# Kernel tuning notes

Measured on AMD Instinct MI355X. Metric: run time of the kernel, lower is better.

Reference implementation:

```python
import jax, jax.numpy as jnp
import numpy as np

B, S, H = 2, 2048, 1024
NH = 16
HD = H // NH
SCALE = 1.0 / np.sqrt(HD).astype(np.float32)


def setup_inputs() -> dict:
    key = jax.random.key(0)
    ks = jax.random.split(key, 7)
    lim = 1.0 / np.sqrt(H)  # lecun-ish init scale for linear weights
    return {
        "query": jax.random.normal(ks[0], (B, S, H), dtype=jnp.float32),
        "key_in": jax.random.normal(ks[1], (B, S, H), dtype=jnp.float32),
        "value": jax.random.normal(ks[2], (B, S, H), dtype=jnp.float32),
        "attention_mask": jnp.ones((B, S), dtype=jnp.int32),
        "Wq": jax.random.uniform(ks[3], (H, H), jnp.float32, -lim, lim),
        "Wk": jax.random.uniform(ks[4], (H, H), jnp.float32, -lim, lim),
        "Wv": jax.random.uniform(ks[5], (H, H), jnp.float32, -lim, lim),
        "Wo": jax.random.uniform(ks[6], (H, H), jnp.float32, -lim, lim),
    }


def reference(query, key_in, value, attention_mask, Wq, Wk, Wv, Wo):
    b, s, _ = query.shape
    # projections (no bias)
    q = (query @ Wq).reshape(b, s, NH, HD).transpose(0, 2, 1, 3)  # [b,h,s,d]
    k = (key_in @ Wk).reshape(b, s, NH, HD).transpose(0, 2, 1, 3)
    v = (value @ Wv).reshape(b, s, NH, HD).transpose(0, 2, 1, 3)

    scores = jnp.einsum("bhqd,bhkd->bhqk", q, k) * SCALE  # [b,h,s,s]
    mask = attention_mask[:, None, None, :]  # broadcast over heads & query pos
    scores = jnp.where(mask == 0, -1e9, scores)
    attn = jax.nn.softmax(scores, axis=-1)

    ctx = jnp.einsum("bhqk,bhkd->bhqd", attn, v)
    ctx = ctx.transpose(0, 2, 1, 3).reshape(b, s, H)
    out = ctx @ Wo
    return out, jnp.mean(attn, axis=1)
```

## Files before the change

### kernel.cpp

```cpp
#include <hip/hip_runtime.h>
#include <stdint.h>

#define BB 2
#define SS 2048
#define HH 1024
#define NHEAD 16
#define HDIM 64

constexpr int   BSROWS = BB * SS;
constexpr float SCALE  = 0.125f;
constexpr float LOG2E  = 1.4426950408889634f;
constexpr float SL     = SCALE * LOG2E;

typedef __bf16 bf16;
typedef __attribute__((ext_vector_type(8))) __bf16 bf16x8;
typedef __attribute__((ext_vector_type(4))) __bf16 bf16x4;
typedef __attribute__((ext_vector_type(4))) float  f32x4;

#define MFMA16(a, b, c) __builtin_amdgcn_mfma_f32_16x16x32_bf16((a), (b), (c), 0, 0, 0)

__device__ __forceinline__ void gload_lds16(const void* g, void* l) {
  __builtin_amdgcn_global_load_lds((const __attribute__((address_space(1))) void*)g,
                                   (__attribute__((address_space(3))) void*)l, 16, 0, 0);
}

__global__ __launch_bounds__(256) void cvt_in(const float* __restrict__ q, const float* __restrict__ k,
                                              const float* __restrict__ v, const int* __restrict__ mask,
                                              bf16* __restrict__ xq, bf16* __restrict__ xk,
                                              bf16* __restrict__ xv, float* __restrict__ bias2) {
  int i = blockIdx.x * 256 + threadIdx.x;
  int e = i * 4;
  f32x4 a = *(const f32x4*)(q + e);
  f32x4 b = *(const f32x4*)(k + e);
  f32x4 c = *(const f32x4*)(v + e);
  *(bf16x4*)(xq + e) = __builtin_convertvector(a, bf16x4);
  *(bf16x4*)(xk + e) = __builtin_convertvector(b, bf16x4);
  *(bf16x4*)(xv + e) = __builtin_convertvector(c, bf16x4);
  if (i < BB * SS) bias2[i] = mask[i] ? 0.0f : -1e9f * LOG2E;
}

__global__ __launch_bounds__(256) void cvt_wt(const float* __restrict__ Wq, const float* __restrict__ Wk,
                                              const float* __restrict__ Wv, const float* __restrict__ Wo,
                                              bf16* __restrict__ Wt) {
  __shared__ float tile[32][33];
  int z = blockIdx.z;
  const float* W = (z == 0) ? Wq : (z == 1) ? Wk : (z == 2) ? Wv : Wo;
  bf16* out = Wt + (size_t)z * HH * HH;
  int bx = blockIdx.x * 32, by = blockIdx.y * 32;
  int tx = threadIdx.x, ty = threadIdx.y;
#pragma unroll
  for (int j = 0; j < 32; j += 8)
    tile[ty + j][tx] = W[(size_t)(by + ty + j) * HH + bx + tx];
  __syncthreads();
#pragma unroll
  for (int j = 0; j < 32; j += 8)
    out[(size_t)(bx + ty + j) * HH + by + tx] = (bf16)tile[tx][ty + j];
}

__global__ __launch_bounds__(256) void gemm128(const bf16* __restrict__ Abase, const bf16* __restrict__ Btbase,
                                               bf16* __restrict__ Qo, bf16* __restrict__ Ko,
                                               bf16* __restrict__ Vto, float* __restrict__ outF, int mode) {
  int id  = blockIdx.x + 8 * blockIdx.y + 256 * blockIdx.z;
  int nwg = 256 * gridDim.z;
  int sw  = (id & 7) * (nwg >> 3) + (id >> 3);
  int bx  = sw & 7, by = (sw >> 3) & 31, bz = sw >> 8;

  int zmode = (mode < 0) ? bz : mode;
  const bf16* A  = Abase  + (mode < 0 ? (size_t)bz * BSROWS * HH : 0);
  const bf16* Bt = Btbase + (mode < 0 ? (size_t)bz * HH * HH : 0);

  __shared__ __align__(16) bf16 lA[2][128 * 32];
  __shared__ __align__(16) bf16 lB[2][128 * 32];

  int t = threadIdx.x;
  int w = t >> 6, l = t & 63, lg = l >> 4, lr = l & 15;
  int m0 = by * 128, n0 = bx * 128;
  int wr = (w >> 1) * 64, wc = (w & 1) * 64;

  f32x4 zero4 = {0.f, 0.f, 0.f, 0.f};
  f32x4 acc[4][4];
#pragma unroll
  for (int i = 0; i < 4; i++)
#pragma unroll
    for (int j = 0; j < 4; j++) acc[i][j] = zero4;

#pragma unroll
  for (int i = 0; i < 2; i++) {
    int idx = i * 256 + t;
    gload_lds16(A  + (size_t)(m0 + (idx >> 2)) * HH + (idx & 3) * 8, &lA[0][(i * 256 + w * 64) * 8]);
    gload_lds16(Bt + (size_t)(n0 + (idx >> 2)) * HH + (idx & 3) * 8, &lB[0][(i * 256 + w * 64) * 8]);
  }
  __syncthreads();

  for (int kt = 0; kt < 32; kt++) {
    int cur = kt & 1;
    if (kt < 31) {
      int kn = (kt + 1) * 32;
#pragma unroll
      for (int i = 0; i < 2; i++) {
        int idx = i * 256 + t;
        gload_lds16(A  + (size_t)(m0 + (idx >> 2)) * HH + kn + (idx & 3) * 8, &lA[cur ^ 1][(i * 256 + w * 64) * 8]);
        gload_lds16(Bt + (size_t)(n0 + (idx >> 2)) * HH + kn + (idx & 3) * 8, &lB[cur ^ 1][(i * 256 + w * 64) * 8]);
      }
    }
    bf16x8 af[4], bq[4];
#pragma unroll
    for (int mi = 0; mi < 4; mi++) af[mi] = *(const bf16x8*)&lA[cur][(wr + mi * 16 + lr) * 32 + lg * 8];
#pragma unroll
    for (int ni = 0; ni < 4; ni++) bq[ni] = *(const bf16x8*)&lB[cur][(wc + ni * 16 + lr) * 32 + lg * 8];
#pragma unroll
    for (int mi = 0; mi < 4; mi++)
#pragma unroll
      for (int ni = 0; ni < 4; ni++)
        acc[mi][ni] = MFMA16(af[mi], bq[ni], acc[mi][ni]);
    __syncthreads();
  }

#pragma unroll
  for (int mi = 0; mi < 4; mi++) {
    int row0 = m0 + wr + mi * 16 + lg * 4;
#pragma unroll
    for (int ni = 0; ni < 4; ni++) {
      int col = n0 + wc + ni * 16 + lr;
      if (zmode == 3) {
#pragma unroll
        for (int r = 0; r < 4; r++) outF[(size_t)(row0 + r) * HH + col] = acc[mi][ni][r];
      } else if (zmode == 2) {
        int b = row0 >> 11, s0 = row0 & (SS - 1);
        int h = col >> 6, d = col & 63;
        bf16x4 pk;
#pragma unroll
        for (int r = 0; r < 4; r++) pk[r] = (bf16)acc[mi][ni][r];
        *(bf16x4*)&Vto[((size_t)(b * NHEAD + h) * HDIM + d) * SS + s0] = pk;
      } else {
        bf16* dst = (zmode == 0) ? Qo : Ko;
        int h = col >> 6, d = col & 63;
#pragma unroll
        for (int r = 0; r < 4; r++) {
          int row = row0 + r;
          int b = row >> 11, s = row & (SS - 1);
          dst[((size_t)(b * NHEAD + h) * SS + s) * HDIM + d] = (bf16)acc[mi][ni][r];
        }
      }
    }
  }
}

__global__ __launch_bounds__(256, 2) void attn_pv(const bf16* __restrict__ Q, const bf16* __restrict__ K,
                                                  const bf16* __restrict__ Vt, const float* __restrict__ bias2,
                                                  float* __restrict__ invl, bf16* __restrict__ ctx) {
  int id = blockIdx.x + 16 * blockIdx.y + 256 * blockIdx.z;
  int sw = (id & 7) * 64 + (id >> 3);
  int b = sw >> 8, h = (sw >> 4) & 15, q0 = (sw & 15) * 128;
  int t = threadIdx.x, w = t >> 6, l = t & 63, lg = l >> 4, lr = l & 15;
  size_t hb = ((size_t)b * NHEAD + h) * SS;
  const bf16* Qh = Q + hb * HDIM;
  const bf16* Kh = K + hb * HDIM;
  const bf16* Vh = Vt + ((size_t)b * NHEAD + h) * HDIM * SS;
  const float* biasb = bias2 + b * SS;

  __shared__ __align__(16) bf16 sK[2][64][72];
  __shared__ __align__(16) bf16 sV[2][64][72];
  __shared__ __align__(16) bf16 lp[4][2][32][72];

  int r0 = t >> 3, c0 = (t & 7) * 8;
  bf16x8 kreg[2], vreg[2];

  int qa = q0 + w * 32;
  int rowa = qa + lr, rowb = qa + 16 + lr;
  bf16x8 qf0a = *(const bf16x8*)&Qh[(size_t)rowa * HDIM + lg * 8];
  bf16x8 qf1a = *(const bf16x8*)&Qh[(size_t)rowa * HDIM + 32 + lg * 8];
  bf16x8 qf0b = *(const bf16x8*)&Qh[(size_t)rowb * HDIM + lg * 8];
  bf16x8 qf1b = *(const bf16x8*)&Qh[(size_t)rowb * HDIM + 32 + lg * 8];

  f32x4 zero4 = {0.f, 0.f, 0.f, 0.f};
  f32x4 lacca = zero4, laccb = zero4;
  f32x4 ctxa[4], ctxb[4];
#pragma unroll
  for (int nd = 0; nd < 4; nd++) { ctxa[nd] = zero4; ctxb[nd] = zero4; }
  bf16x8 vh[2][4];

#pragma unroll
  for (int i = 0; i < 2; i++) {
    int row = i * 32 + r0;
    kreg[i] = *(const bf16x8*)&Kh[(size_t)row * HDIM + c0];
    vreg[i] = *(const bf16x8*)&Vh[(size_t)row * SS + c0];
  }
#pragma unroll
  for (int i = 0; i < 2; i++) {
    int row = i * 32 + r0;
    *(bf16x8*)&sK[0][row][c0] = kreg[i];
    *(bf16x8*)&sV[0][row][c0] = vreg[i];
  }
  __syncthreads();

  for (int kt = 0; kt < 32; kt++) {
    int k0 = kt * 64, cur = kt & 1, prev = cur ^ 1;
    if (kt < 31) {
      int kn = k0 + 64;
#pragma unroll
      for (int i = 0; i < 2; i++) {
        int row = i * 32 + r0;
        kreg[i] = *(const bf16x8*)&Kh[(size_t)(kn + row) * HDIM + c0];
        vreg[i] = *(const bf16x8*)&Vh[(size_t)row * SS + kn + c0];
      }
    }
    if (kt > 0) {
#pragma unroll
      for (int kk = 0; kk < 2; kk++) {
        bf16x8 paa = *(const bf16x8*)&lp[w][prev][lr][kk * 32 + lg * 8];
        bf16x8 pab = *(const bf16x8*)&lp[w][prev][16 + lr][kk * 32 + lg * 8];
#pragma unroll
        for (int nd = 0; nd < 4; nd++) {
          ctxa[nd] = MFMA16(paa, vh[kk][nd], ctxa[nd]);
          ctxb[nd] = MFMA16(pab, vh[kk][nd], ctxb[nd]);
        }
      }
    }
    f32x4 acca[4], accb[4];
#pragma unroll
    for (int ni = 0; ni < 4; ni++) {
      const bf16* kp = &sK[cur][ni * 16 + lr][lg * 8];
      bf16x8 kf0 = *(const bf16x8*)kp;
      bf16x8 kf1 = *(const bf16x8*)(kp + 32);
      acca[ni] = MFMA16(kf1, qf1a, MFMA16(kf0, qf0a, zero4));
      accb[ni] = MFMA16(kf1, qf1b, MFMA16(kf0, qf0b, zero4));
    }
#pragma unroll
    for (int kk = 0; kk < 2; kk++)
#pragma unroll
      for (int nd = 0; nd < 4; nd++)
        vh[kk][nd] = *(const bf16x8*)&sV[cur][nd * 16 + lr][kk * 32 + lg * 8];
    f32x4 pa4[4], pb4[4];
#pragma unroll
    for (int ni = 0; ni < 4; ni++) {
      f32x4 bv = *(const f32x4*)&biasb[k0 + ni * 16 + lg * 4];
      f32x4 za = acca[ni] * SL + bv;
      f32x4 zb = accb[ni] * SL + bv;
#pragma unroll
      for (int r = 0; r < 4; r++) {
        pa4[ni][r] = __builtin_amdgcn_exp2f(za[r]);
        pb4[ni][r] = __builtin_amdgcn_exp2f(zb[r]);
      }
    }
    lacca += (pa4[0] + pa4[1]) + (pa4[2] + pa4[3]);
    laccb += (pb4[0] + pb4[1]) + (pb4[2] + pb4[3]);
#pragma unroll
    for (int ni = 0; ni < 4; ni++) {
      *(bf16x4*)&lp[w][cur][lr][ni * 16 + lg * 4]      = __builtin_convertvector(pa4[ni], bf16x4);
      *(bf16x4*)&lp[w][cur][16 + lr][ni * 16 + lg * 4] = __builtin_convertvector(pb4[ni], bf16x4);
    }
    if (kt < 31) {
#pragma unroll
      for (int i = 0; i < 2; i++) {
        int row = i * 32 + r0;
        *(bf16x8*)&sK[prev][row][c0] = kreg[i];
        *(bf16x8*)&sV[prev][row][c0] = vreg[i];
      }
      __syncthreads();
    }
  }

#pragma unroll
  for (int kk = 0; kk < 2; kk++) {
    bf16x8 paa = *(const bf16x8*)&lp[w][1][lr][kk * 32 + lg * 8];
    bf16x8 pab = *(const bf16x8*)&lp[w][1][16 + lr][kk * 32 + lg * 8];
#pragma unroll
    for (int nd = 0; nd < 4; nd++) {
      ctxa[nd] = MFMA16(paa, vh[kk][nd], ctxa[nd]);
      ctxb[nd] = MFMA16(pab, vh[kk][nd], ctxb[nd]);
    }
  }

  float lsa = (lacca[0] + lacca[1]) + (lacca[2] + lacca[3]);
  float lsb = (laccb[0] + laccb[1]) + (laccb[2] + laccb[3]);
  lsa += __shfl_xor(lsa, 16); lsa += __shfl_xor(lsa, 32);
  lsb += __shfl_xor(lsb, 16); lsb += __shfl_xor(lsb, 32);
  float ila = 1.0f / lsa, ilb = 1.0f / lsb;
  f32x4 ilva, ilvb;
#pragma unroll
  for (int r = 0; r < 4; r++) { ilva[r] = __shfl(ila, lg * 4 + r); ilvb[r] = __shfl(ilb, lg * 4 + r); }
#pragma unroll
  for (int nd = 0; nd < 4; nd++)
#pragma unroll
    for (int r = 0; r < 4; r++) {
      int ra = qa + lg * 4 + r, rb = qa + 16 + lg * 4 + r;
      ctx[(size_t)(b * SS + ra) * HH + h * HDIM + nd * 16 + lr] = (bf16)(ctxa[nd][r] * ilva[r]);
      ctx[(size_t)(b * SS + rb) * HH + h * HDIM + nd * 16 + lr] = (bf16)(ctxb[nd][r] * ilvb[r]);
    }
  if (l < 16) {
    invl[hb + qa + l]      = ila;
    invl[hb + qa + 16 + l] = ilb;
  }
}

__global__ __launch_bounds__(256, 4) void attn_mean(const bf16* __restrict__ Q, const bf16* __restrict__ K,
                                                    const float* __restrict__ bias2,
                                                    const float* __restrict__ invl, float* __restrict__ meanOut) {
  int id = blockIdx.x + 16 * blockIdx.y + 512 * blockIdx.z;
  int sw = (id & 7) * 128 + (id >> 3);
  int b = sw >> 9, kc0 = ((sw >> 4) & 31) * 64, q0 = (sw & 15) * 128;
  int t = threadIdx.x, w = t >> 6, l = t & 63, lg = l >> 4, lr = l & 15;
  const float* biasb = bias2 + b * SS;
  __shared__ __align__(16) bf16 sK[2][64][64];

  int rloc = l >> 3;
  int csw  = (l & 7) ^ (rloc & 7);
  int swz  = lr & 7;

  int qa = q0 + w * 32;
  int rowa = qa + lr, rowb = qa + 16 + lr;

  f32x4 bv[4];
#pragma unroll
  for (int ni = 0; ni < 4; ni++) bv[ni] = *(const f32x4*)&biasb[kc0 + ni * 16 + lg * 4];

  f32x4 zero4 = {0.f, 0.f, 0.f, 0.f};
  f32x4 macca[4], maccb[4];
#pragma unroll
  for (int ni = 0; ni < 4; ni++) { macca[ni] = zero4; maccb[ni] = zero4; }

  bf16x8 qf0a, qf1a, qf0b, qf1b;
  float ila, ilb;
  {
    const bf16* Kh0 = K + ((size_t)b * NHEAD) * SS * HDIM;
#pragma unroll
    for (int i = 0; i < 2; i++) {
      int rs = w * 16 + i * 8;
      gload_lds16(Kh0 + (size_t)(kc0 + rs + rloc) * HDIM + csw * 8, &sK[0][rs][0]);
    }
    const bf16* Qh0 = Q + ((size_t)b * NHEAD) * SS * HDIM;
    qf0a = *(const bf16x8*)&Qh0[(size_t)rowa * HDIM + lg * 8];
    qf1a = *(const bf16x8*)&Qh0[(size_t)rowa * HDIM + 32 + lg * 8];
    qf0b = *(const bf16x8*)&Qh0[(size_t)rowb * HDIM + lg * 8];
    qf1b = *(const bf16x8*)&Qh0[(size_t)rowb * HDIM + 32 + lg * 8];
    size_t hb0 = (size_t)b * NHEAD * SS;
    ila = invl[hb0 + rowa] * (1.0f / NHEAD);
    ilb = invl[hb0 + rowb] * (1.0f / NHEAD);
  }
  __syncthreads();

  for (int h = 0; h < NHEAD; h++) {
    int cur = h & 1;
    bf16x8 qn0a, qn1a, qn0b, qn1b;
    float ina = 0.f, inb = 0.f;
    if (h < NHEAD - 1) {
      size_t hbn = ((size_t)b * NHEAD + h + 1) * SS;
      const bf16* Khn = K + hbn * HDIM;
#pragma unroll
      for (int i = 0; i < 2; i++) {
        int rs = w * 16 + i * 8;
        gload_lds16(Khn + (size_t)(kc0 + rs + rloc) * HDIM + csw * 8, &sK[cur ^ 1][rs][0]);
      }
      const bf16* Qhn = Q + hbn * HDIM;
      qn0a = *(const bf16x8*)&Qhn[(size_t)rowa * HDIM + lg * 8];
      qn1a = *(const bf16x8*)&Qhn[(size_t)rowa * HDIM + 32 + lg * 8];
      qn0b = *(const bf16x8*)&Qhn[(size_t)rowb * HDIM + lg * 8];
      qn1b = *(const bf16x8*)&Qhn[(size_t)rowb * HDIM + 32 + lg * 8];
      ina = invl[hbn + rowa] * (1.0f / NHEAD);
      inb = invl[hbn + rowb] * (1.0f / NHEAD);
    }
#pragma unroll
    for (int ni = 0; ni < 4; ni++) {
      bf16x8 kf0 = *(const bf16x8*)&sK[cur][ni * 16 + lr][(lg ^ swz) * 8];
      bf16x8 kf1 = *(const bf16x8*)&sK[cur][ni * 16 + lr][((4 + lg) ^ swz) * 8];
      f32x4 acca = MFMA16(kf1, qf1a, MFMA16(kf0, qf0a, zero4));
      f32x4 accb = MFMA16(kf1, qf1b, MFMA16(kf0, qf0b, zero4));
      f32x4 za = acca * SL + bv[ni];
      f32x4 zb = accb * SL + bv[ni];
#pragma unroll
      for (int r = 0; r < 4; r++) {
        macca[ni][r] += __builtin_amdgcn_exp2f(za[r]) * ila;
        maccb[ni][r] += __builtin_amdgcn_exp2f(zb[r]) * ilb;
      }
    }
    if (h < NHEAD - 1) {
      qf0a = qn0a; qf1a = qn1a; qf0b = qn0b; qf1b = qn1b;
      ila = ina; ilb = inb;
      __syncthreads();
    }
  }
  float* meanB = meanOut + (size_t)b * SS * SS;
#pragma unroll
  for (int ni = 0; ni < 4; ni++) {
    *(f32x4*)&meanB[(size_t)rowa * SS + kc0 + ni * 16 + lg * 4] = macca[ni];
    *(f32x4*)&meanB[(size_t)rowb * SS + kc0 + ni * 16 + lg * 4] = maccb[ni];
  }
}

extern "C" void kernel_launch(void* const* d_in, const int* in_sizes, int n_in,
                              void* d_out, int out_size, void* d_ws, size_t ws_size,
                              hipStream_t stream) {
  const float* query  = (const float*)d_in[0];
  const float* key_in = (const float*)d_in[1];
  const float* value  = (const float*)d_in[2];
  const int*   mask   = (const int*)d_in[3];
  const float* Wq     = (const float*)d_in[4];
  const float* Wk     = (const float*)d_in[5];
  const float* Wv     = (const float*)d_in[6];
  const float* Wo     = (const float*)d_in[7];

  char* ws = (char*)d_ws;
  bf16*  Xb    = (bf16*)(ws);
  bf16*  Wt    = (bf16*)(ws + 25165824);
  bf16*  Qb    = (bf16*)(ws + 33554432);
  bf16*  Kb    = (bf16*)(ws + 41943040);
  bf16*  Vtb   = (bf16*)(ws + 50331648);
  float* invlb = (float*)(ws + 58982400);
  float* biasb = (float*)(ws + 59244544);
  bf16*  ctxb  = Xb;

  float* outF  = (float*)d_out;
  float* meanF = outF + (size_t)BB * SS * HH;

  cvt_in<<<4096, 256, 0, stream>>>(query, key_in, value, mask,
                                   Xb, Xb + 4194304, Xb + 8388608, biasb);
  cvt_wt<<<dim3(32, 32, 4), dim3(32, 8), 0, stream>>>(Wq, Wk, Wv, Wo, Wt);
  gemm128<<<dim3(8, 32, 3), 256, 0, stream>>>(Xb, Wt, Qb, Kb, Vtb, nullptr, -1);
  attn_pv<<<dim3(16, 16, 2), 256, 0, stream>>>(Qb, Kb, Vtb, biasb, invlb, ctxb);
  attn_mean<<<dim3(16, 32, 2), 256, 0, stream>>>(Qb, Kb, biasb, invlb, meanF);
  gemm128<<<dim3(8, 32, 1), 256, 0, stream>>>(ctxb, Wt + 3 * (size_t)HH * HH,
                                              nullptr, nullptr, nullptr, outF, 3);
}
```

Before: 178.6 us.

## Give each attention wave 64 query rows with 2 waves per block

```diff
diff --git a/kernel.cpp b/kernel.cpp
--- a/kernel.cpp
+++ b/kernel.cpp
@@ -146,9 +146,9 @@
   }
 }
 
-__global__ __launch_bounds__(256, 2) void attn_pv(const bf16* __restrict__ Q, const bf16* __restrict__ K,
-                                                  const bf16* __restrict__ Vt, const float* __restrict__ bias2,
-                                                  float* __restrict__ invl, bf16* __restrict__ ctx) {
+__global__ __launch_bounds__(128) void attn_pv(const bf16* __restrict__ Q, const bf16* __restrict__ K,
+                                               const bf16* __restrict__ Vt, const float* __restrict__ bias2,
+                                               float* __restrict__ invl, bf16* __restrict__ ctx) {
   int id = blockIdx.x + 16 * blockIdx.y + 256 * blockIdx.z;
   int sw = (id & 7) * 64 + (id >> 3);
   int b = sw >> 8, h = (sw >> 4) & 15, q0 = (sw & 15) * 128;
@@ -161,36 +161,44 @@
 
   __shared__ __align__(16) bf16 sK[2][64][72];
   __shared__ __align__(16) bf16 sV[2][64][72];
-  __shared__ __align__(16) bf16 lp[4][2][32][72];
+  __shared__ __align__(16) bf16 lp[2][2][64][72];
 
   int r0 = t >> 3, c0 = (t & 7) * 8;
-  bf16x8 kreg[2], vreg[2];
-
-  int qa = q0 + w * 32;
-  int rowa = qa + lr, rowb = qa + 16 + lr;
-  bf16x8 qf0a = *(const bf16x8*)&Qh[(size_t)rowa * HDIM + lg * 8];
-  bf16x8 qf1a = *(const bf16x8*)&Qh[(size_t)rowa * HDIM + 32 + lg * 8];
-  bf16x8 qf0b = *(const bf16x8*)&Qh[(size_t)rowb * HDIM + lg * 8];
-  bf16x8 qf1b = *(const bf16x8*)&Qh[(size_t)rowb * HDIM + 32 + lg * 8];
+  bf16x8 kreg[4], vreg[4];
+
+  int qa = q0 + w * 64;
+  bf16x8 qf0[4], qf1[4];
+#pragma unroll
+  for (int c = 0; c < 4; c++) {
+    int rowc = qa + c * 16 + lr;
+    qf0[c] = *(const bf16x8*)&Qh[(size_t)rowc * HDIM + lg * 8];
+    qf1[c] = *(const bf16x8*)&Qh[(size_t)rowc * HDIM + 32 + lg * 8];
+  }
 
   f32x4 zero4 = {0.f, 0.f, 0.f, 0.f};
-  f32x4 lacca = zero4, laccb = zero4;
-  f32x4 ctxa[4], ctxb[4];
-#pragma unroll
-  for (int nd = 0; nd < 4; nd++) { ctxa[nd] = zero4; ctxb[nd] = zero4; }
+  f32x4 lacc[4];
+  f32x4 ctxc[4][4];
+#pragma unroll
+  for (int c = 0; c < 4; c++) {
+    lacc[c] = zero4;
+#pragma unroll
+    for (int nd = 0; nd < 4; nd++) ctxc[c][nd] = zero4;
+  }
   bf16x8 vh[2][4];
 
 #pragma unroll
-  for (int i = 0; i < 2; i++) {
-    int row = i * 32 + r0;
-    kreg[i] = *(const bf16x8*)&Kh[(size_t)row * HDIM + c0];
-    vreg[i] = *(const bf16x8*)&Vh[(size_t)row * SS + c0];
-  }
-#pragma unroll
-  for (int i = 0; i < 2; i++) {
-    int row = i * 32 + r0;
-    *(bf16x8*)&sK[0][row][c0] = kreg[i];
-    *(bf16x8*)&sV[0][row][c0] = vreg[i];
+  for (int i = 0; i < 4; i++) {
+    int idx = i * 128 + t;
+    int row = idx >> 3, col = (idx & 7) * 8;
+    kreg[i] = *(const bf16x8*)&Kh[(size_t)row * HDIM + col];
+    vreg[i] = *(const bf16x8*)&Vh[(size_t)row * SS + col];
+  }
+#pragma unroll
+  for (int i = 0; i < 4; i++) {
+    int idx = i * 128 + t;
+    int row = idx >> 3, col = (idx & 7) * 8;
+    *(bf16x8*)&sK[0][row][col] = kreg[i];
+    *(bf16x8*)&sV[0][row][col] = vreg[i];
   }
   __syncthreads();
 
@@ -199,98 +207,90 @@
     if (kt < 31) {
       int kn = k0 + 64;
 #pragma unroll
-      for (int i = 0; i < 2; i++) {
-        int row = i * 32 + r0;
-        kreg[i] = *(const bf16x8*)&Kh[(size_t)(kn + row) * HDIM + c0];
-        vreg[i] = *(const bf16x8*)&Vh[(size_t)row * SS + kn + c0];
+      for (int i = 0; i < 4; i++) {
+        int idx = i * 128 + t;
+        int row = idx >> 3, col = (idx & 7) * 8;
+        kreg[i] = *(const bf16x8*)&Kh[(size_t)(kn + row) * HDIM + col];
+        vreg[i] = *(const bf16x8*)&Vh[(size_t)row * SS + kn + col];
       }
     }
     if (kt > 0) {
 #pragma unroll
-      for (int kk = 0; kk < 2; kk++) {
-        bf16x8 paa = *(const bf16x8*)&lp[w][prev][lr][kk * 32 + lg * 8];
-        bf16x8 pab = *(const bf16x8*)&lp[w][prev][16 + lr][kk * 32 + lg * 8];
-#pragma unroll
-        for (int nd = 0; nd < 4; nd++) {
-          ctxa[nd] = MFMA16(paa, vh[kk][nd], ctxa[nd]);
-          ctxb[nd] = MFMA16(pab, vh[kk][nd], ctxb[nd]);
+      for (int kk = 0; kk < 2; kk++)
+#pragma unroll
+        for (int c = 0; c < 4; c++) {
+          bf16x8 pac = *(const bf16x8*)&lp[w][prev][c * 16 + lr][kk * 32 + lg * 8];
+#pragma unroll
+          for (int nd = 0; nd < 4; nd++)
+            ctxc[c][nd] = MFMA16(pac, vh[kk][nd], ctxc[c][nd]);
         }
-      }
-    }
-    f32x4 acca[4], accb[4];
+    }
+    f32x4 acc[4][4];
 #pragma unroll
     for (int ni = 0; ni < 4; ni++) {
       const bf16* kp = &sK[cur][ni * 16 + lr][lg * 8];
       bf16x8 kf0 = *(const bf16x8*)kp;
       bf16x8 kf1 = *(const bf16x8*)(kp + 32);
-      acca[ni] = MFMA16(kf1, qf1a, MFMA16(kf0, qf0a, zero4));
-      accb[ni] = MFMA16(kf1, qf1b, MFMA16(kf0, qf0b, zero4));
+#pragma unroll
+      for (int c = 0; c < 4; c++)
+        acc[c][ni] = MFMA16(kf1, qf1[c], MFMA16(kf0, qf0[c], zero4));
     }
 #pragma unroll
     for (int kk = 0; kk < 2; kk++)
 #pragma unroll
       for (int nd = 0; nd < 4; nd++)
         vh[kk][nd] = *(const bf16x8*)&sV[cur][nd * 16 + lr][kk * 32 + lg * 8];
-    f32x4 pa4[4], pb4[4];
 #pragma unroll
     for (int ni = 0; ni < 4; ni++) {
       f32x4 bv = *(const f32x4*)&biasb[k0 + ni * 16 + lg * 4];
-      f32x4 za = acca[ni] * SL + bv;
-      f32x4 zb = accb[ni] * SL + bv;
+#pragma unroll
+      for (int c = 0; c < 4; c++) {
+        f32x4 z = acc[c][ni] * SL + bv;
+        f32x4 p;
+#pragma unroll
+        for (int r = 0; r < 4; r++) p[r] = __builtin_amdgcn_exp2f(z[r]);
+        lacc[c] += p;
+        *(bf16x4*)&lp[w][cur][c * 16 + lr][ni * 16 + lg * 4] = __builtin_convertvector(p, bf16x4);
+      }
+    }
+    if (kt < 31) {
+#pragma unroll
+      for (int i = 0; i < 4; i++) {
+        int idx = i * 128 + t;
+        int row = idx >> 3, col = (idx & 7) * 8;
+        *(bf16x8*)&sK[prev][row][col] = kreg[i];
+        *(bf16x8*)&sV[prev][row][col] = vreg[i];
+      }
+      __syncthreads();
+    }
+  }
+
+#pragma unroll
+  for (int kk = 0; kk < 2; kk++)
+#pragma unroll
+    for (int c = 0; c < 4; c++) {
+      bf16x8 pac = *(const bf16x8*)&lp[w][1][c * 16 + lr][kk * 32 + lg * 8];
+#pragma unroll
+      for (int nd = 0; nd < 4; nd++)
+        ctxc[c][nd] = MFMA16(pac, vh[kk][nd], ctxc[c][nd]);
+    }
+
+#pragma unroll
+  for (int c = 0; c < 4; c++) {
+    float ls = (lacc[c][0] + lacc[c][1]) + (lacc[c][2] + lacc[c][3]);
+    ls += __shfl_xor(ls, 16); ls += __shfl_xor(ls, 32);
+    float il = 1.0f / ls;
+    f32x4 ilv;
+#pragma unroll
+    for (int r = 0; r < 4; r++) ilv[r] = __shfl(il, lg * 4 + r);
+#pragma unroll
+    for (int nd = 0; nd < 4; nd++)
 #pragma unroll
       for (int r = 0; r < 4; r++) {
-        pa4[ni][r] = __builtin_amdgcn_exp2f(za[r]);
-        pb4[ni][r] = __builtin_amdgcn_exp2f(zb[r]);
-      }
-    }
-    lacca += (pa4[0] + pa4[1]) + (pa4[2] + pa4[3]);
-    laccb += (pb4[0] + pb4[1]) + (pb4[2] + pb4[3]);
-#pragma unroll
-    for (int ni = 0; ni < 4; ni++) {
-      *(bf16x4*)&lp[w][cur][lr][ni * 16 + lg * 4]      = __builtin_convertvector(pa4[ni], bf16x4);
-      *(bf16x4*)&lp[w][cur][16 + lr][ni * 16 + lg * 4] = __builtin_convertvector(pb4[ni], bf16x4);
-    }
-    if (kt < 31) {
-#pragma unroll
-      for (int i = 0; i < 2; i++) {
-        int row = i * 32 + r0;
-        *(bf16x8*)&sK[prev][row][c0] = kreg[i];
-        *(bf16x8*)&sV[prev][row][c0] = vreg[i];
-      }
-      __syncthreads();
-    }
-  }
-
-#pragma unroll
-  for (int kk = 0; kk < 2; kk++) {
-    bf16x8 paa = *(const bf16x8*)&lp[w][1][lr][kk * 32 + lg * 8];
-    bf16x8 pab = *(const bf16x8*)&lp[w][1][16 + lr][kk * 32 + lg * 8];
-#pragma unroll
-    for (int nd = 0; nd < 4; nd++) {
-      ctxa[nd] = MFMA16(paa, vh[kk][nd], ctxa[nd]);
-      ctxb[nd] = MFMA16(pab, vh[kk][nd], ctxb[nd]);
-    }
-  }
-
-  float lsa = (lacca[0] + lacca[1]) + (lacca[2] + lacca[3]);
-  float lsb = (laccb[0] + laccb[1]) + (laccb[2] + laccb[3]);
-  lsa += __shfl_xor(lsa, 16); lsa += __shfl_xor(lsa, 32);
-  lsb += __shfl_xor(lsb, 16); lsb += __shfl_xor(lsb, 32);
-  float ila = 1.0f / lsa, ilb = 1.0f / lsb;
-  f32x4 ilva, ilvb;
-#pragma unroll
-  for (int r = 0; r < 4; r++) { ilva[r] = __shfl(ila, lg * 4 + r); ilvb[r] = __shfl(ilb, lg * 4 + r); }
-#pragma unroll
-  for (int nd = 0; nd < 4; nd++)
-#pragma unroll
-    for (int r = 0; r < 4; r++) {
-      int ra = qa + lg * 4 + r, rb = qa + 16 + lg * 4 + r;
-      ctx[(size_t)(b * SS + ra) * HH + h * HDIM + nd * 16 + lr] = (bf16)(ctxa[nd][r] * ilva[r]);
-      ctx[(size_t)(b * SS + rb) * HH + h * HDIM + nd * 16 + lr] = (bf16)(ctxb[nd][r] * ilvb[r]);
-    }
-  if (l < 16) {
-    invl[hb + qa + l]      = ila;
-    invl[hb + qa + 16 + l] = ilb;
+        int row = qa + c * 16 + lg * 4 + r;
+        ctx[(size_t)(b * SS + row) * HH + h * HDIM + nd * 16 + lr] = (bf16)(ctxc[c][nd][r] * ilv[r]);
+      }
+    if (l < 16) invl[hb + qa + c * 16 + l] = il;
   }
 }
 
@@ -417,7 +417,7 @@
                                    Xb, Xb + 4194304, Xb + 8388608, biasb);
   cvt_wt<<<dim3(32, 32, 4), dim3(32, 8), 0, stream>>>(Wq, Wk, Wv, Wo, Wt);
   gemm128<<<dim3(8, 32, 3), 256, 0, stream>>>(Xb, Wt, Qb, Kb, Vtb, nullptr, -1);
-  attn_pv<<<dim3(16, 16, 2), 256, 0, stream>>>(Qb, Kb, Vtb, biasb, invlb, ctxb);
+  attn_pv<<<dim3(16, 16, 2), 128, 0, stream>>>(Qb, Kb, Vtb, biasb, invlb, ctxb);
   attn_mean<<<dim3(16, 32, 2), 256, 0, stream>>>(Qb, Kb, biasb, invlb, meanF);
   gemm128<<<dim3(8, 32, 1), 256, 0, stream>>>(ctxb, Wt + 3 * (size_t)HH * HH,
                                               nullptr, nullptr, nullptr, outF, 3);
```

Result: slower. 209.4 us, median of 2 (+17.2%).
